# Kernel tuning notes

Hardware: AMD Instinct MI355X
Metric: run time of the kernel (lower is better)

Reference implementation:

```python
import jax, jax.numpy as jnp
import numpy as np

D, DK, DV = 1024, 128, 128
N = 8192


def setup_inputs() -> dict:
    key = jax.random.key(0)
    ks = jax.random.split(key, 7)
    s = 1.0 / np.sqrt(D)
    return {
        "X": jax.random.normal(ks[0], (N, D), dtype=jnp.float32),
        "Wq": jax.random.uniform(ks[1], (D, DK), jnp.float32, -s, s),
        "bq": jax.random.uniform(ks[2], (DK,), jnp.float32, -s, s),
        "Wk": jax.random.uniform(ks[3], (D, DK), jnp.float32, -s, s),
        "bk": jax.random.uniform(ks[4], (DK,), jnp.float32, -s, s),
        "Wv": jax.random.uniform(ks[5], (D, DV), jnp.float32, -s, s),
        "bv": jax.random.uniform(ks[6], (DV,), jnp.float32, -s, s),
    }


def reference(X, Wq, bq, Wk, bk, Wv, bv):
    # Projections (torch Linear: y = x @ W^T + b; here W stored as [in, out])
    Q = X @ Wq + bq            # [N, d_k]
    K = X @ Wk + bk            # [N, d_k]
    V = X @ Wv + bv            # [N, d_v]
    n, d_k = Q.shape
    scores = (Q @ K.T) / jnp.sqrt(jnp.asarray(d_k, Q.dtype))  # [N, N]
    # Causal mask: positions j > i get -inf before softmax
    causal = jnp.tril(jnp.ones((n, n), dtype=bool))
    scores = jnp.where(causal, scores, -jnp.inf)
    weights = jax.nn.softmax(scores, axis=-1)  # [N, N]
    return weights @ V          # [N, d_v]
```

## Files before the change

### kernel.cpp

```cpp
#include <hip/hip_runtime.h>
#include <hip/hip_bf16.h>

#define N_TOK 8192
#define D_IN  1024
#define DK    128
#define NT    256

typedef __attribute__((ext_vector_type(8))) short short8;
typedef __attribute__((ext_vector_type(4))) float f32x4;

static __device__ __forceinline__ unsigned short f2bf(float f) {
    __hip_bfloat16 h = __float2bfloat16(f);
    return __builtin_bit_cast(unsigned short, h);
}

static __device__ __forceinline__ void gl_lds16(const void* g, void* l) {
    __builtin_amdgcn_global_load_lds(
        (const __attribute__((address_space(1))) void*)g,
        (__attribute__((address_space(3))) void*)l, 16, 0, 0);
}

__global__ __launch_bounds__(256) void wtrans_kernel(
    const float* __restrict__ Wq, const float* __restrict__ Wk,
    const float* __restrict__ Wv, unsigned short* __restrict__ Wt)
{
    __shared__ unsigned short T[64][72];
    const int proj = blockIdx.y;
    const float* W = (proj == 0) ? Wq : (proj == 1) ? Wk : Wv;
    unsigned short* out = Wt + (size_t)proj * DK * D_IN;
    const int k0 = (blockIdx.x & 15) * 64, n0 = (blockIdx.x >> 4) * 64;
    const int tid = threadIdx.x;
    #pragma unroll
    for (int i = 0; i < 4; i++) {
        int e = tid + i * 256;
        int r = e >> 4, c4 = e & 15;
        float4 v = *reinterpret_cast<const float4*>(&W[(size_t)(k0 + r) * DK + n0 + c4 * 4]);
        T[c4 * 4 + 0][r] = f2bf(v.x);
        T[c4 * 4 + 1][r] = f2bf(v.y);
        T[c4 * 4 + 2][r] = f2bf(v.z);
        T[c4 * 4 + 3][r] = f2bf(v.w);
    }
    __syncthreads();
    #pragma unroll
    for (int i = 0; i < 4; i++) {
        int e = tid + i * 256;
        int r = e >> 4, c4 = e & 15;
        *reinterpret_cast<ushort4*>(&out[(size_t)(n0 + r) * D_IN + k0 + c4 * 4]) =
            *reinterpret_cast<const ushort4*>(&T[r][c4 * 4]);
    }
}

__global__ __launch_bounds__(256) void proj_fused(
    const float* __restrict__ X, const unsigned short* __restrict__ Wt,
    const float* __restrict__ bq, const float* __restrict__ bk,
    const float* __restrict__ bv,
    unsigned short* __restrict__ Qb, unsigned short* __restrict__ Kb,
    unsigned short* __restrict__ Vt)
{
    __shared__ unsigned short Xs[2][32][72];

    const int tid = threadIdx.x;
    const int wid = tid >> 6, lane = tid & 63;
    const int g = lane >> 4, r16 = lane & 15;
    const int mb = blockIdx.x * 32;

    float4 xr[2];
    auto XLOAD = [&](int k0) {
        #pragma unroll
        for (int i = 0; i < 2; i++) {
            int e = tid + i * 256;
            int r = e >> 4, c4 = e & 15;
            xr[i] = *reinterpret_cast<const float4*>(
                &X[(size_t)(mb + r) * D_IN + k0 + c4 * 4]);
        }
    };
    auto XWRITE = [&](int buf) {
        #pragma unroll
        for (int i = 0; i < 2; i++) {
            int e = tid + i * 256;
            int r = e >> 4, c4 = e & 15;
            ushort4 h;
            h.x = f2bf(xr[i].x); h.y = f2bf(xr[i].y);
            h.z = f2bf(xr[i].z); h.w = f2bf(xr[i].w);
            *reinterpret_cast<ushort4*>(&Xs[buf][r][c4 * 4]) = h;
        }
    };

    f32x4 acc[2][6] = {};

    XLOAD(0); XWRITE(0);
    __syncthreads();
    for (int s = 0; s < 16; ++s) {
        const int k0 = s * 64;
        const int cur = s & 1;
        if (s + 1 < 16) XLOAD(k0 + 64);
        #pragma unroll
        for (int kk = 0; kk < 64; kk += 32) {
            short8 af[2], bfr[6];
            #pragma unroll
            for (int mi = 0; mi < 2; mi++)
                af[mi] = *reinterpret_cast<const short8*>(&Xs[cur][mi * 16 + r16][kk + g * 8]);
            #pragma unroll
            for (int ni = 0; ni < 6; ni++) {
                int nn = wid * 96 + ni * 16;
                int pj = nn >> 7;
                bfr[ni] = *reinterpret_cast<const short8*>(
                    &Wt[((size_t)pj * DK + (nn & 127) + r16) * D_IN + k0 + kk + g * 8]);
            }
            __builtin_amdgcn_s_setprio(1);
            #pragma unroll
            for (int mi = 0; mi < 2; mi++)
                #pragma unroll
                for (int ni = 0; ni < 6; ni++)
                    acc[mi][ni] = __builtin_amdgcn_mfma_f32_16x16x32_bf16(
                        af[mi], bfr[ni], acc[mi][ni], 0, 0, 0);
            __builtin_amdgcn_s_setprio(0);
        }
        if (s + 1 < 16) XWRITE((s + 1) & 1);
        __syncthreads();
    }

    #pragma unroll
    for (int ni = 0; ni < 6; ni++) {
        int nn = wid * 96 + ni * 16;
        int pj = nn >> 7;
        int n = (nn & 127) + r16;
        const float* bias = (pj == 0) ? bq : (pj == 1) ? bk : bv;
        float b = bias[n];
        if (pj < 2) {
            unsigned short* out = (pj == 0) ? Qb : Kb;
            #pragma unroll
            for (int mi = 0; mi < 2; mi++)
                #pragma unroll
                for (int e = 0; e < 4; e++) {
                    int m = mb + mi * 16 + g * 4 + e;
                    int nc = n;
                    if (pj == 1)
                        nc = ((((n >> 3) ^ (m & 7)) << 3) | (n & 7));
                    out[(size_t)m * DK + nc] = f2bf(acc[mi][ni][e] + b);
                }
        } else {
            #pragma unroll
            for (int mi = 0; mi < 2; mi++) {
                int m0 = mb + mi * 16 + g * 4;
                int mblk = (((m0 & 31) >> 3) ^ (n & 3));
                int mp = (m0 & ~31) | (mblk << 3) | (m0 & 7);
                ushort4 h;
                h.x = f2bf(acc[mi][ni][0] + b);
                h.y = f2bf(acc[mi][ni][1] + b);
                h.z = f2bf(acc[mi][ni][2] + b);
                h.w = f2bf(acc[mi][ni][3] + b);
                *reinterpret_cast<ushort4*>(&Vt[(size_t)n * N_TOK + mp]) = h;
            }
        }
    }
}

__global__ __launch_bounds__(256, 3) void attn_partial(
    const unsigned short* __restrict__ Qb, const unsigned short* __restrict__ Ksw,
    const unsigned short* __restrict__ Vsw,
    float* __restrict__ Opart, float* __restrict__ Mpart, float* __restrict__ Lpart,
    float* __restrict__ O, int chunk_tiles, int max_chunks, int direct)
{
    __shared__ unsigned short Klds[2][32][128];
    __shared__ unsigned short Vlds[2][128][32];
    __shared__ unsigned short Pq[4][32][36];

    const int qb = blockIdx.x, c = blockIdx.y;
    const int j0 = c * chunk_tiles;
    const int jmax = 4 * qb + 4;
    const int jend = min(j0 + chunk_tiles, jmax);
    if (j0 >= jend) return;
    const int nt = jend - j0;

    const int tid = threadIdx.x;
    const int wid = tid >> 6, lane = tid & 63;
    const int g = lane >> 4, r16 = lane & 15;
    const int t = qb * 4 + wid;
    const int qw = t * 32;
    const float scale2 = 0.08838834764831845f * 1.4426950408889634f;

    auto STAGE = [&](int buf, int kvb) {
        #pragma unroll
        for (int s = 0; s < 2; s++) {
            int ob = ((wid * 2 + s) << 10);
            gl_lds16((const char*)Ksw + ((size_t)kvb << 8) + ob + (lane << 4),
                     (char*)&Klds[buf][0][0] + ob);
        }
        #pragma unroll
        for (int s = 0; s < 2; s++) {
            int ob = ((wid * 2 + s) << 10);
            int o = ob + (lane << 4);
            int d = o >> 6, cb = o & 63;
            gl_lds16((const char*)Vsw + (((size_t)d * N_TOK + kvb) << 1) + cb,
                     (char*)&Vlds[buf][0][0] + ob);
        }
    };

    short8 qf[2][4];
    #pragma unroll
    for (int mi = 0; mi < 2; mi++)
        #pragma unroll
        for (int kd = 0; kd < 4; kd++)
            qf[mi][kd] = *reinterpret_cast<const short8*>(
                &Qb[(size_t)(qw + mi * 16 + r16) * DK + kd * 32 + g * 8]);

    f32x4 o_acc[2][8] = {};
    float m_run[2] = {-1e30f, -1e30f}, l_run[2] = {0.f, 0.f};

    STAGE(0, j0 * 32);

    int cur = 0;
    for (int it = 0; it < nt; ++it) {
        const int kvb = (j0 + it) * 32;
        if (it + 1 < nt) {
            STAGE(cur ^ 1, kvb + 32);
            asm volatile("s_waitcnt vmcnt(4)" ::: "memory");
        } else {
            asm volatile("s_waitcnt vmcnt(0)" ::: "memory");
        }
        __builtin_amdgcn_sched_barrier(0);
        __builtin_amdgcn_s_barrier();
        __builtin_amdgcn_sched_barrier(0);

        const unsigned short* Kl = &Klds[cur][0][0];
        const unsigned short* Vl = &Vlds[cur][0][0];

        f32x4 st[2][2] = {};
        #pragma unroll
        for (int kd = 0; kd < 4; kd++) {
            int swb = ((((kd << 2) | g) ^ (r16 & 7)) << 3);
            short8 kf0 = *reinterpret_cast<const short8*>(Kl + r16 * 128 + swb);
            short8 kf1 = *reinterpret_cast<const short8*>(Kl + (16 + r16) * 128 + swb);
            __builtin_amdgcn_s_setprio(1);
            st[0][0] = __builtin_amdgcn_mfma_f32_16x16x32_bf16(kf0, qf[0][kd], st[0][0], 0, 0, 0);
            st[0][1] = __builtin_amdgcn_mfma_f32_16x16x32_bf16(kf0, qf[1][kd], st[0][1], 0, 0, 0);
            st[1][0] = __builtin_amdgcn_mfma_f32_16x16x32_bf16(kf1, qf[0][kd], st[1][0], 0, 0, 0);
            st[1][1] = __builtin_amdgcn_mfma_f32_16x16x32_bf16(kf1, qf[1][kd], st[1][1], 0, 0, 0);
            __builtin_amdgcn_s_setprio(0);
        }

        const bool anymask = (kvb + 31 > qw);
        float alpha[2];
        #pragma unroll
        for (int mi = 0; mi < 2; mi++) {
            const int qrow = qw + mi * 16 + r16;
            float s[2][4];
            #pragma unroll
            for (int ni = 0; ni < 2; ni++)
                #pragma unroll
                for (int e = 0; e < 4; e++) {
                    float v = st[ni][mi][e] * scale2;
                    if (anymask && (kvb + ni * 16 + g * 4 + e > qrow)) v = -1e30f;
                    s[ni][e] = v;
                }
            float lm = fmaxf(fmaxf(fmaxf(s[0][0], s[0][1]), fmaxf(s[0][2], s[0][3])),
                             fmaxf(fmaxf(s[1][0], s[1][1]), fmaxf(s[1][2], s[1][3])));
            lm = fmaxf(lm, __shfl_xor(lm, 16));
            lm = fmaxf(lm, __shfl_xor(lm, 32));
            float mnew = fmaxf(m_run[mi], lm);
            alpha[mi] = exp2f(m_run[mi] - mnew);
            float ps[2][4], ls;
            #pragma unroll
            for (int ni = 0; ni < 2; ni++)
                #pragma unroll
                for (int e = 0; e < 4; e++)
                    ps[ni][e] = exp2f(s[ni][e] - mnew);
            ls = ((ps[0][0] + ps[0][1]) + (ps[0][2] + ps[0][3]))
               + ((ps[1][0] + ps[1][1]) + (ps[1][2] + ps[1][3]));
            ls += __shfl_xor(ls, 16);
            ls += __shfl_xor(ls, 32);
            l_run[mi] = l_run[mi] * alpha[mi] + ls;
            m_run[mi] = mnew;
            #pragma unroll
            for (int ni = 0; ni < 2; ni++) {
                ushort4 pk;
                pk.x = f2bf(ps[ni][0]); pk.y = f2bf(ps[ni][1]);
                pk.z = f2bf(ps[ni][2]); pk.w = f2bf(ps[ni][3]);
                *reinterpret_cast<ushort4*>(&Pq[wid][mi * 16 + r16][ni * 16 + g * 4]) = pk;
            }
        }
        if (__any(alpha[0] < 1.f) || __any(alpha[1] < 1.f)) {
            #pragma unroll
            for (int mi = 0; mi < 2; mi++)
                #pragma unroll
                for (int df = 0; df < 8; df++)
                    #pragma unroll
                    for (int e = 0; e < 4; e++)
                        o_acc[mi][df][e] *= alpha[mi];
        }
        short8 pb0 = *reinterpret_cast<const short8*>(&Pq[wid][r16][g * 8]);
        short8 pb1 = *reinterpret_cast<const short8*>(&Pq[wid][16 + r16][g * 8]);
        const int swv = ((g ^ (r16 & 3)) << 3);
        #pragma unroll
        for (int df = 0; df < 8; df++) {
            short8 vf = *reinterpret_cast<const short8*>(Vl + (df * 16 + r16) * 32 + swv);
            __builtin_amdgcn_s_setprio(1);
            o_acc[0][df] = __builtin_amdgcn_mfma_f32_16x16x32_bf16(vf, pb0, o_acc[0][df], 0, 0, 0);
            o_acc[1][df] = __builtin_amdgcn_mfma_f32_16x16x32_bf16(vf, pb1, o_acc[1][df], 0, 0, 0);
            __builtin_amdgcn_s_setprio(0);
        }

        __builtin_amdgcn_sched_barrier(0);
        __builtin_amdgcn_s_barrier();
        __builtin_amdgcn_sched_barrier(0);
        cur ^= 1;
    }

    if (direct) {
        #pragma unroll
        for (int mi = 0; mi < 2; mi++) {
            float inv = 1.0f / l_run[mi];
            #pragma unroll
            for (int df = 0; df < 8; df++) {
                f32x4 r = o_acc[mi][df];
                r[0] *= inv; r[1] *= inv; r[2] *= inv; r[3] *= inv;
                *reinterpret_cast<f32x4*>(
                    &O[(size_t)(qw + mi * 16 + r16) * DK + df * 16 + g * 4]) = r;
            }
        }
    } else {
        size_t pb0i = ((size_t)t * max_chunks + c) * 32;
        #pragma unroll
        for (int mi = 0; mi < 2; mi++) {
            #pragma unroll
            for (int df = 0; df < 8; df++)
                *reinterpret_cast<f32x4*>(
                    &Opart[(pb0i + mi * 16 + r16) * 128 + df * 16 + g * 4]) = o_acc[mi][df];
            if (g == 0) {
                Mpart[pb0i + mi * 16 + r16] = m_run[mi];
                Lpart[pb0i + mi * 16 + r16] = l_run[mi];
            }
        }
    }
}

__global__ __launch_bounds__(256) void attn_merge(
    const float* __restrict__ Opart, const float* __restrict__ Mpart,
    const float* __restrict__ Lpart, float* __restrict__ O,
    int chunk_tiles, int max_chunks)
{
    __shared__ float Ms[32], Ls[32], Fs[16][32];
    const int t = blockIdx.x;
    const int nc = t / chunk_tiles + 1;
    const int tid = threadIdx.x;

    if (tid < 32) {
        float M = -1e30f;
        for (int c = 0; c < nc; c++)
            M = fmaxf(M, Mpart[((size_t)t * max_chunks + c) * 32 + tid]);
        float L = 0.f;
        for (int c = 0; c < nc; c++) {
            size_t pb = ((size_t)t * max_chunks + c) * 32 + tid;
            L += exp2f(Mpart[pb] - M) * Lpart[pb];
        }
        Ms[tid] = M; Ls[tid] = L;
    }
    __syncthreads();
    for (int cc = tid >> 5; cc < nc; cc += 8) {
        int row = tid & 31;
        Fs[cc][row] = exp2f(Mpart[((size_t)t * max_chunks + cc) * 32 + row] - Ms[row]);
    }
    __syncthreads();
    #pragma unroll
    for (int it = 0; it < 4; it++) {
        int idx = tid + it * 256;
        int row = idx >> 5, c4 = idx & 31;
        float4 acc = {0.f, 0.f, 0.f, 0.f};
        for (int c = 0; c < nc; c++) {
            const float4 v = *reinterpret_cast<const float4*>(
                &Opart[(((size_t)t * max_chunks + c) * 32 + row) * 128 + c4 * 4]);
            float f = Fs[c][row];
            acc.x += f * v.x; acc.y += f * v.y; acc.z += f * v.z; acc.w += f * v.w;
        }
        float inv = 1.0f / Ls[row];
        float4 r;
        r.x = acc.x * inv; r.y = acc.y * inv; r.z = acc.z * inv; r.w = acc.w * inv;
        *reinterpret_cast<float4*>(&O[((size_t)t * 32 + row) * DK + c4 * 4]) = r;
    }
}

extern "C" void kernel_launch(void* const* d_in, const int* in_sizes, int n_in,
                              void* d_out, int out_size, void* d_ws, size_t ws_size,
                              hipStream_t stream) {
    const float* X  = (const float*)d_in[0];
    const float* Wq = (const float*)d_in[1];
    const float* bq = (const float*)d_in[2];
    const float* Wk = (const float*)d_in[3];
    const float* bk = (const float*)d_in[4];
    const float* Wv = (const float*)d_in[5];
    const float* bv = (const float*)d_in[6];
    float* O = (float*)d_out;

    unsigned short* Qb = (unsigned short*)d_ws;
    unsigned short* Kb = Qb + (size_t)N_TOK * DK;
    unsigned short* Vt = Kb + (size_t)N_TOK * DK;
    unsigned short* Wt = Vt + (size_t)N_TOK * DK;
    float* Opart = (float*)(Wt + (size_t)3 * DK * D_IN);
    size_t base_bytes = (size_t)((char*)Opart - (char*)d_ws);

    int chunk_tiles = 0, max_chunks = 1, direct = 0;
    const int opts[4] = {16, 32, 64, 128};
    for (int i = 0; i < 4; i++) {
        int ct = opts[i], mc = NT / ct;
        size_t need = base_bytes + (size_t)NT * mc * 32 * (128 + 2) * sizeof(float);
        if (need <= ws_size) { chunk_tiles = ct; max_chunks = mc; break; }
    }
    if (!chunk_tiles) { chunk_tiles = NT; max_chunks = 1; direct = 1; }
    float* Mpart = Opart + (size_t)NT * max_chunks * 32 * 128;
    float* Lpart = Mpart + (size_t)NT * max_chunks * 32;

    wtrans_kernel<<<dim3(32, 3), 256, 0, stream>>>(Wq, Wk, Wv, Wt);
    proj_fused<<<dim3(256), 256, 0, stream>>>(X, Wt, bq, bk, bv, Qb, Kb, Vt);
    int grid_c = direct ? 1 : max_chunks;
    attn_partial<<<dim3(64, grid_c), 256, 0, stream>>>(
        Qb, Kb, Vt, Opart, Mpart, Lpart, O, chunk_tiles, max_chunks, direct);
    if (!direct)
        attn_merge<<<dim3(NT), 256, 0, stream>>>(Opart, Mpart, Lpart, O,
                                                 chunk_tiles, max_chunks);
}
```

Before: 112.4 us.

## Halve per-wave query tile to 16 rows, doubling blocks in projection and attention

The projection and attention kernels now give each wave 16 query rows instead of 32, so twice as many blocks are launched and each block's causal range is shorter. Register use drops (one MFMA row-tile instead of two), and attn_partial raises its launch bound from 3 to 4 blocks per SIMD. The merge kernel is re-indexed to 16-row tiles. The trade-off is that every staged K/V tile feeds half as many MFMAs, so K/V traffic from global memory and LDS per unit of compute doubles.

Measured after the change: 128.0 us. 13.9% more time.

```diff
diff --git a/kernel.cpp b/kernel.cpp
--- a/kernel.cpp
+++ b/kernel.cpp
@@ -4,7 +4,8 @@
 #define N_TOK 8192
 #define D_IN  1024
 #define DK    128
-#define NT    256
+#define NKV   256
+#define NT16  512
 
 typedef __attribute__((ext_vector_type(8))) short short8;
 typedef __attribute__((ext_vector_type(4))) float f32x4;
@@ -57,36 +58,28 @@
     unsigned short* __restrict__ Qb, unsigned short* __restrict__ Kb,
     unsigned short* __restrict__ Vt)
 {
-    __shared__ unsigned short Xs[2][32][72];
+    __shared__ unsigned short Xs[2][16][72];
 
     const int tid = threadIdx.x;
     const int wid = tid >> 6, lane = tid & 63;
     const int g = lane >> 4, r16 = lane & 15;
-    const int mb = blockIdx.x * 32;
-
-    float4 xr[2];
+    const int mb = blockIdx.x * 16;
+
+    float4 xr;
     auto XLOAD = [&](int k0) {
-        #pragma unroll
-        for (int i = 0; i < 2; i++) {
-            int e = tid + i * 256;
-            int r = e >> 4, c4 = e & 15;
-            xr[i] = *reinterpret_cast<const float4*>(
-                &X[(size_t)(mb + r) * D_IN + k0 + c4 * 4]);
-        }
+        int r = tid >> 4, c4 = tid & 15;
+        xr = *reinterpret_cast<const float4*>(
+            &X[(size_t)(mb + r) * D_IN + k0 + c4 * 4]);
     };
     auto XWRITE = [&](int buf) {
-        #pragma unroll
-        for (int i = 0; i < 2; i++) {
-            int e = tid + i * 256;
-            int r = e >> 4, c4 = e & 15;
-            ushort4 h;
-            h.x = f2bf(xr[i].x); h.y = f2bf(xr[i].y);
-            h.z = f2bf(xr[i].z); h.w = f2bf(xr[i].w);
-            *reinterpret_cast<ushort4*>(&Xs[buf][r][c4 * 4]) = h;
-        }
+        int r = tid >> 4, c4 = tid & 15;
+        ushort4 h;
+        h.x = f2bf(xr.x); h.y = f2bf(xr.y);
+        h.z = f2bf(xr.z); h.w = f2bf(xr.w);
+        *reinterpret_cast<ushort4*>(&Xs[buf][r][c4 * 4]) = h;
     };
 
-    f32x4 acc[2][6] = {};
+    f32x4 acc[6] = {};
 
     XLOAD(0); XWRITE(0);
     __syncthreads();
@@ -96,10 +89,8 @@
         if (s + 1 < 16) XLOAD(k0 + 64);
         #pragma unroll
         for (int kk = 0; kk < 64; kk += 32) {
-            short8 af[2], bfr[6];
-            #pragma unroll
-            for (int mi = 0; mi < 2; mi++)
-                af[mi] = *reinterpret_cast<const short8*>(&Xs[cur][mi * 16 + r16][kk + g * 8]);
+            short8 af = *reinterpret_cast<const short8*>(&Xs[cur][r16][kk + g * 8]);
+            short8 bfr[6];
             #pragma unroll
             for (int ni = 0; ni < 6; ni++) {
                 int nn = wid * 96 + ni * 16;
@@ -109,11 +100,9 @@
             }
             __builtin_amdgcn_s_setprio(1);
             #pragma unroll
-            for (int mi = 0; mi < 2; mi++)
-                #pragma unroll
-                for (int ni = 0; ni < 6; ni++)
-                    acc[mi][ni] = __builtin_amdgcn_mfma_f32_16x16x32_bf16(
-                        af[mi], bfr[ni], acc[mi][ni], 0, 0, 0);
+            for (int ni = 0; ni < 6; ni++)
+                acc[ni] = __builtin_amdgcn_mfma_f32_16x16x32_bf16(
+                    af, bfr[ni], acc[ni], 0, 0, 0);
             __builtin_amdgcn_s_setprio(0);
         }
         if (s + 1 < 16) XWRITE((s + 1) & 1);
@@ -130,33 +119,28 @@
         if (pj < 2) {
             unsigned short* out = (pj == 0) ? Qb : Kb;
             #pragma unroll
-            for (int mi = 0; mi < 2; mi++)
-                #pragma unroll
-                for (int e = 0; e < 4; e++) {
-                    int m = mb + mi * 16 + g * 4 + e;
-                    int nc = n;
-                    if (pj == 1)
-                        nc = ((((n >> 3) ^ (m & 7)) << 3) | (n & 7));
-                    out[(size_t)m * DK + nc] = f2bf(acc[mi][ni][e] + b);
-                }
+            for (int e = 0; e < 4; e++) {
+                int m = mb + g * 4 + e;
+                int nc = n;
+                if (pj == 1)
+                    nc = ((((n >> 3) ^ (m & 7)) << 3) | (n & 7));
+                out[(size_t)m * DK + nc] = f2bf(acc[ni][e] + b);
+            }
         } else {
-            #pragma unroll
-            for (int mi = 0; mi < 2; mi++) {
-                int m0 = mb + mi * 16 + g * 4;
-                int mblk = (((m0 & 31) >> 3) ^ (n & 3));
-                int mp = (m0 & ~31) | (mblk << 3) | (m0 & 7);
-                ushort4 h;
-                h.x = f2bf(acc[mi][ni][0] + b);
-                h.y = f2bf(acc[mi][ni][1] + b);
-                h.z = f2bf(acc[mi][ni][2] + b);
-                h.w = f2bf(acc[mi][ni][3] + b);
-                *reinterpret_cast<ushort4*>(&Vt[(size_t)n * N_TOK + mp]) = h;
-            }
-        }
-    }
-}
-
-__global__ __launch_bounds__(256, 3) void attn_partial(
+            int m0 = mb + g * 4;
+            int mblk = (((m0 & 31) >> 3) ^ (n & 3));
+            int mp = (m0 & ~31) | (mblk << 3) | (m0 & 7);
+            ushort4 h;
+            h.x = f2bf(acc[ni][0] + b);
+            h.y = f2bf(acc[ni][1] + b);
+            h.z = f2bf(acc[ni][2] + b);
+            h.w = f2bf(acc[ni][3] + b);
+            *reinterpret_cast<ushort4*>(&Vt[(size_t)n * N_TOK + mp]) = h;
+        }
+    }
+}
+
+__global__ __launch_bounds__(256, 4) void attn_partial(
     const unsigned short* __restrict__ Qb, const unsigned short* __restrict__ Ksw,
     const unsigned short* __restrict__ Vsw,
     float* __restrict__ Opart, float* __restrict__ Mpart, float* __restrict__ Lpart,
@@ -164,11 +148,11 @@
 {
     __shared__ unsigned short Klds[2][32][128];
     __shared__ unsigned short Vlds[2][128][32];
-    __shared__ unsigned short Pq[4][32][36];
+    __shared__ unsigned short Pq[4][16][36];
 
     const int qb = blockIdx.x, c = blockIdx.y;
     const int j0 = c * chunk_tiles;
-    const int jmax = 4 * qb + 4;
+    const int jmax = 2 * qb + 2;
     const int jend = min(j0 + chunk_tiles, jmax);
     if (j0 >= jend) return;
     const int nt = jend - j0;
@@ -176,8 +160,8 @@
     const int tid = threadIdx.x;
     const int wid = tid >> 6, lane = tid & 63;
     const int g = lane >> 4, r16 = lane & 15;
-    const int t = qb * 4 + wid;
-    const int qw = t * 32;
+    const int t16 = qb * 4 + wid;
+    const int qw = t16 * 16;
     const float scale2 = 0.08838834764831845f * 1.4426950408889634f;
 
     auto STAGE = [&](int buf, int kvb) {
@@ -197,16 +181,14 @@
         }
     };
 
-    short8 qf[2][4];
-    #pragma unroll
-    for (int mi = 0; mi < 2; mi++)
-        #pragma unroll
-        for (int kd = 0; kd < 4; kd++)
-            qf[mi][kd] = *reinterpret_cast<const short8*>(
-                &Qb[(size_t)(qw + mi * 16 + r16) * DK + kd * 32 + g * 8]);
-
-    f32x4 o_acc[2][8] = {};
-    float m_run[2] = {-1e30f, -1e30f}, l_run[2] = {0.f, 0.f};
+    short8 qf[4];
+    #pragma unroll
+    for (int kd = 0; kd < 4; kd++)
+        qf[kd] = *reinterpret_cast<const short8*>(
+            &Qb[(size_t)(qw + r16) * DK + kd * 32 + g * 8]);
+
+    f32x4 o_acc[8] = {};
+    float m_run = -1e30f, l_run = 0.f;
 
     STAGE(0, j0 * 32);
 
@@ -226,78 +208,68 @@
         const unsigned short* Kl = &Klds[cur][0][0];
         const unsigned short* Vl = &Vlds[cur][0][0];
 
-        f32x4 st[2][2] = {};
+        f32x4 st[2] = {};
         #pragma unroll
         for (int kd = 0; kd < 4; kd++) {
             int swb = ((((kd << 2) | g) ^ (r16 & 7)) << 3);
             short8 kf0 = *reinterpret_cast<const short8*>(Kl + r16 * 128 + swb);
             short8 kf1 = *reinterpret_cast<const short8*>(Kl + (16 + r16) * 128 + swb);
             __builtin_amdgcn_s_setprio(1);
-            st[0][0] = __builtin_amdgcn_mfma_f32_16x16x32_bf16(kf0, qf[0][kd], st[0][0], 0, 0, 0);
-            st[0][1] = __builtin_amdgcn_mfma_f32_16x16x32_bf16(kf0, qf[1][kd], st[0][1], 0, 0, 0);
-            st[1][0] = __builtin_amdgcn_mfma_f32_16x16x32_bf16(kf1, qf[0][kd], st[1][0], 0, 0, 0);
-            st[1][1] = __builtin_amdgcn_mfma_f32_16x16x32_bf16(kf1, qf[1][kd], st[1][1], 0, 0, 0);
+            st[0] = __builtin_amdgcn_mfma_f32_16x16x32_bf16(kf0, qf[kd], st[0], 0, 0, 0);
+            st[1] = __builtin_amdgcn_mfma_f32_16x16x32_bf16(kf1, qf[kd], st[1], 0, 0, 0);
             __builtin_amdgcn_s_setprio(0);
         }
 
         const bool anymask = (kvb + 31 > qw);
-        float alpha[2];
-        #pragma unroll
-        for (int mi = 0; mi < 2; mi++) {
-            const int qrow = qw + mi * 16 + r16;
-            float s[2][4];
-            #pragma unroll
-            for (int ni = 0; ni < 2; ni++)
-                #pragma unroll
-                for (int e = 0; e < 4; e++) {
-                    float v = st[ni][mi][e] * scale2;
-                    if (anymask && (kvb + ni * 16 + g * 4 + e > qrow)) v = -1e30f;
-                    s[ni][e] = v;
-                }
-            float lm = fmaxf(fmaxf(fmaxf(s[0][0], s[0][1]), fmaxf(s[0][2], s[0][3])),
-                             fmaxf(fmaxf(s[1][0], s[1][1]), fmaxf(s[1][2], s[1][3])));
-            lm = fmaxf(lm, __shfl_xor(lm, 16));
-            lm = fmaxf(lm, __shfl_xor(lm, 32));
-            float mnew = fmaxf(m_run[mi], lm);
-            alpha[mi] = exp2f(m_run[mi] - mnew);
-            float ps[2][4], ls;
-            #pragma unroll
-            for (int ni = 0; ni < 2; ni++)
+        const int qrow = qw + r16;
+        float s[2][4];
+        #pragma unroll
+        for (int ni = 0; ni < 2; ni++)
+            #pragma unroll
+            for (int e = 0; e < 4; e++) {
+                float v = st[ni][e] * scale2;
+                if (anymask && (kvb + ni * 16 + g * 4 + e > qrow)) v = -1e30f;
+                s[ni][e] = v;
+            }
+        float lm = fmaxf(fmaxf(fmaxf(s[0][0], s[0][1]), fmaxf(s[0][2], s[0][3])),
+                         fmaxf(fmaxf(s[1][0], s[1][1]), fmaxf(s[1][2], s[1][3])));
+        lm = fmaxf(lm, __shfl_xor(lm, 16));
+        lm = fmaxf(lm, __shfl_xor(lm, 32));
+        float mnew = fmaxf(m_run, lm);
+        float alpha = exp2f(m_run - mnew);
+        float ps[2][4], ls;
+        #pragma unroll
+        for (int ni = 0; ni < 2; ni++)
+            #pragma unroll
+            for (int e = 0; e < 4; e++)
+                ps[ni][e] = exp2f(s[ni][e] - mnew);
+        ls = ((ps[0][0] + ps[0][1]) + (ps[0][2] + ps[0][3]))
+           + ((ps[1][0] + ps[1][1]) + (ps[1][2] + ps[1][3]));
+        ls += __shfl_xor(ls, 16);
+        ls += __shfl_xor(ls, 32);
+        l_run = l_run * alpha + ls;
+        m_run = mnew;
+        #pragma unroll
+        for (int ni = 0; ni < 2; ni++) {
+            ushort4 pk;
+            pk.x = f2bf(ps[ni][0]); pk.y = f2bf(ps[ni][1]);
+            pk.z = f2bf(ps[ni][2]); pk.w = f2bf(ps[ni][3]);
+            *reinterpret_cast<ushort4*>(&Pq[wid][r16][ni * 16 + g * 4]) = pk;
+        }
+        if (__any(alpha < 1.f)) {
+            #pragma unroll
+            for (int df = 0; df < 8; df++)
                 #pragma unroll
                 for (int e = 0; e < 4; e++)
-                    ps[ni][e] = exp2f(s[ni][e] - mnew);
-            ls = ((ps[0][0] + ps[0][1]) + (ps[0][2] + ps[0][3]))
-               + ((ps[1][0] + ps[1][1]) + (ps[1][2] + ps[1][3]));
-            ls += __shfl_xor(ls, 16);
-            ls += __shfl_xor(ls, 32);
-            l_run[mi] = l_run[mi] * alpha[mi] + ls;
-            m_run[mi] = mnew;
-            #pragma unroll
-            for (int ni = 0; ni < 2; ni++) {
-                ushort4 pk;
-                pk.x = f2bf(ps[ni][0]); pk.y = f2bf(ps[ni][1]);
-                pk.z = f2bf(ps[ni][2]); pk.w = f2bf(ps[ni][3]);
-                *reinterpret_cast<ushort4*>(&Pq[wid][mi * 16 + r16][ni * 16 + g * 4]) = pk;
-            }
-        }
-        if (__any(alpha[0] < 1.f) || __any(alpha[1] < 1.f)) {
-            #pragma unroll
-            for (int mi = 0; mi < 2; mi++)
-                #pragma unroll
-                for (int df = 0; df < 8; df++)
-                    #pragma unroll
-                    for (int e = 0; e < 4; e++)
-                        o_acc[mi][df][e] *= alpha[mi];
-        }
-        short8 pb0 = *reinterpret_cast<const short8*>(&Pq[wid][r16][g * 8]);
-        short8 pb1 = *reinterpret_cast<const short8*>(&Pq[wid][16 + r16][g * 8]);
+                    o_acc[df][e] *= alpha;
+        }
+        short8 pbf = *reinterpret_cast<const short8*>(&Pq[wid][r16][g * 8]);
         const int swv = ((g ^ (r16 & 3)) << 3);
         #pragma unroll
         for (int df = 0; df < 8; df++) {
             short8 vf = *reinterpret_cast<const short8*>(Vl + (df * 16 + r16) * 32 + swv);
             __builtin_amdgcn_s_setprio(1);
-            o_acc[0][df] = __builtin_amdgcn_mfma_f32_16x16x32_bf16(vf, pb0, o_acc[0][df], 0, 0, 0);
-            o_acc[1][df] = __builtin_amdgcn_mfma_f32_16x16x32_bf16(vf, pb1, o_acc[1][df], 0, 0, 0);
+            o_acc[df] = __builtin_amdgcn_mfma_f32_16x16x32_bf16(vf, pbf, o_acc[df], 0, 0, 0);
             __builtin_amdgcn_s_setprio(0);
         }
 
@@ -308,29 +280,23 @@
     }
 
     if (direct) {
-        #pragma unroll
-        for (int mi = 0; mi < 2; mi++) {
-            float inv = 1.0f / l_run[mi];
-            #pragma unroll
-            for (int df = 0; df < 8; df++) {
-                f32x4 r = o_acc[mi][df];
-                r[0] *= inv; r[1] *= inv; r[2] *= inv; r[3] *= inv;
-                *reinterpret_cast<f32x4*>(
-                    &O[(size_t)(qw + mi * 16 + r16) * DK + df * 16 + g * 4]) = r;
-            }
+        float inv = 1.0f / l_run;
+        #pragma unroll
+        for (int df = 0; df < 8; df++) {
+            f32x4 r = o_acc[df];
+            r[0] *= inv; r[1] *= inv; r[2] *= inv; r[3] *= inv;
+            *reinterpret_cast<f32x4*>(
+                &O[(size_t)(qw + r16) * DK + df * 16 + g * 4]) = r;
         }
     } else {
-        size_t pb0i = ((size_t)t * max_chunks + c) * 32;
-        #pragma unroll
-        for (int mi = 0; mi < 2; mi++) {
-            #pragma unroll
-            for (int df = 0; df < 8; df++)
-                *reinterpret_cast<f32x4*>(
-                    &Opart[(pb0i + mi * 16 + r16) * 128 + df * 16 + g * 4]) = o_acc[mi][df];
-            if (g == 0) {
-                Mpart[pb0i + mi * 16 + r16] = m_run[mi];
-                Lpart[pb0i + mi * 16 + r16] = l_run[mi];
-            }
+        size_t pb0i = ((size_t)t16 * max_chunks + c) * 16;
+        #pragma unroll
+        for (int df = 0; df < 8; df++)
+            *reinterpret_cast<f32x4*>(
+                &Opart[(pb0i + r16) * 128 + df * 16 + g * 4]) = o_acc[df];
+        if (g == 0) {
+            Mpart[pb0i + r16] = m_run;
+            Lpart[pb0i + r16] = l_run;
         }
     }
 }
@@ -340,43 +306,45 @@
     const float* __restrict__ Lpart, float* __restrict__ O,
     int chunk_tiles, int max_chunks)
 {
-    __shared__ float Ms[32], Ls[32], Fs[16][32];
-    const int t = blockIdx.x;
-    const int nc = t / chunk_tiles + 1;
+    __shared__ float Ms[16], Ls[16], Fs[16][16];
+    const int t16 = blockIdx.x;
+    const int kv_tiles = (t16 >> 1) + 1;
+    const int nc = (kv_tiles + chunk_tiles - 1) / chunk_tiles;
     const int tid = threadIdx.x;
 
-    if (tid < 32) {
+    if (tid < 16) {
         float M = -1e30f;
         for (int c = 0; c < nc; c++)
-            M = fmaxf(M, Mpart[((size_t)t * max_chunks + c) * 32 + tid]);
+            M = fmaxf(M, Mpart[((size_t)t16 * max_chunks + c) * 16 + tid]);
         float L = 0.f;
         for (int c = 0; c < nc; c++) {
-            size_t pb = ((size_t)t * max_chunks + c) * 32 + tid;
+            size_t pb = ((size_t)t16 * max_chunks + c) * 16 + tid;
             L += exp2f(Mpart[pb] - M) * Lpart[pb];
         }
         Ms[tid] = M; Ls[tid] = L;
     }
     __syncthreads();
-    for (int cc = tid >> 5; cc < nc; cc += 8) {
-        int row = tid & 31;
-        Fs[cc][row] = exp2f(Mpart[((size_t)t * max_chunks + cc) * 32 + row] - Ms[row]);
+    {
+        int cc = tid >> 4, row = tid & 15;
+        if (cc < nc)
+            Fs[cc][row] = exp2f(Mpart[((size_t)t16 * max_chunks + cc) * 16 + row] - Ms[row]);
     }
     __syncthreads();
     #pragma unroll
-    for (int it = 0; it < 4; it++) {
+    for (int it = 0; it < 2; it++) {
         int idx = tid + it * 256;
         int row = idx >> 5, c4 = idx & 31;
         float4 acc = {0.f, 0.f, 0.f, 0.f};
         for (int c = 0; c < nc; c++) {
             const float4 v = *reinterpret_cast<const float4*>(
-                &Opart[(((size_t)t * max_chunks + c) * 32 + row) * 128 + c4 * 4]);
+                &Opart[(((size_t)t16 * max_chunks + c) * 16 + row) * 128 + c4 * 4]);
             float f = Fs[c][row];
             acc.x += f * v.x; acc.y += f * v.y; acc.z += f * v.z; acc.w += f * v.w;
         }
         float inv = 1.0f / Ls[row];
         float4 r;
         r.x = acc.x * inv; r.y = acc.y * inv; r.z = acc.z * inv; r.w = acc.w * inv;
-        *reinterpret_cast<float4*>(&O[((size_t)t * 32 + row) * DK + c4 * 4]) = r;
+        *reinterpret_cast<float4*>(&O[((size_t)t16 * 16 + row) * DK + c4 * 4]) = r;
     }
 }
 
@@ -402,20 +370,20 @@
     int chunk_tiles = 0, max_chunks = 1, direct = 0;
     const int opts[4] = {16, 32, 64, 128};
     for (int i = 0; i < 4; i++) {
-        int ct = opts[i], mc = NT / ct;
-        size_t need = base_bytes + (size_t)NT * mc * 32 * (128 + 2) * sizeof(float);
+        int ct = opts[i], mc = NKV / ct;
+        size_t need = base_bytes + (size_t)NT16 * mc * 16 * (128 + 2) * sizeof(float);
         if (need <= ws_size) { chunk_tiles = ct; max_chunks = mc; break; }
     }
-    if (!chunk_tiles) { chunk_tiles = NT; max_chunks = 1; direct = 1; }
-    float* Mpart = Opart + (size_t)NT * max_chunks * 32 * 128;
-    float* Lpart = Mpart + (size_t)NT * max_chunks * 32;
+    if (!chunk_tiles) { chunk_tiles = NKV; max_chunks = 1; direct = 1; }
+    float* Mpart = Opart + (size_t)NT16 * max_chunks * 16 * 128;
+    float* Lpart = Mpart + (size_t)NT16 * max_chunks * 16;
 
     wtrans_kernel<<<dim3(32, 3), 256, 0, stream>>>(Wq, Wk, Wv, Wt);
-    proj_fused<<<dim3(256), 256, 0, stream>>>(X, Wt, bq, bk, bv, Qb, Kb, Vt);
+    proj_fused<<<dim3(512), 256, 0, stream>>>(X, Wt, bq, bk, bv, Qb, Kb, Vt);
     int grid_c = direct ? 1 : max_chunks;
-    attn_partial<<<dim3(64, grid_c), 256, 0, stream>>>(
+    attn_partial<<<dim3(128, grid_c), 256, 0, stream>>>(
         Qb, Kb, Vt, Opart, Mpart, Lpart, O, chunk_tiles, max_chunks, direct);
     if (!direct)
-        attn_merge<<<dim3(NT), 256, 0, stream>>>(Opart, Mpart, Lpart, O,
-                                                 chunk_tiles, max_chunks);
-}
+        attn_merge<<<dim3(NT16), 256, 0, stream>>>(Opart, Mpart, Lpart, O,
+                                                   chunk_tiles, max_chunks);
+}
```
